# Performance work log

Measured on AMD Instinct MI355X. Metric: run time of the kernel, lower is better.

Reference implementation:

```python
import jax, jax.numpy as jnp
import numpy as np

L, H, DK = 4, 8, 64
NEG = -1e9
PAD = -9999.0


def _ln(z, g, b, eps=1e-6):
    # LayerNormalization: uses unbiased std (torch default) and divides by (std + eps)
    m = jnp.mean(z, axis=-1, keepdims=True)
    s = jnp.std(z, axis=-1, keepdims=True, ddof=1)
    return g * (z - m) / (s + eps) + b


def _mha(q_in, kv_in, w, bw, pw, pb, lnp, mask):
    B, Sq, D = q_in.shape
    q = (q_in @ w[0] + bw[0]).reshape(B, Sq, H, DK).transpose(0, 2, 1, 3)
    k = (kv_in @ w[1] + bw[1]).reshape(B, -1, H, DK).transpose(0, 2, 1, 3)
    v = (kv_in @ w[2] + bw[2]).reshape(B, -1, H, DK).transpose(0, 2, 1, 3)
    scores = jnp.einsum('bhqd,bhkd->bhqk', q, k) * (1.0 / np.sqrt(DK))
    if mask is not None:
        scores = jnp.where(mask[:, None, :, :], NEG, scores)
    attn = jax.nn.softmax(scores, axis=-1)
    ctx = jnp.einsum('bhqk,bhkd->bhqd', attn, v).transpose(0, 2, 1, 3).reshape(B, Sq, H * DK)
    return _ln(q_in + ctx @ pw + pb, lnp[0], lnp[1])


def _ffn(x, w1, b1, w2, b2, lnp):
    # kernel-1 conv1d == pointwise linear; w1:[d_ff,d_model], w2:[d_model,d_ff]
    h = jax.nn.relu(jnp.einsum('bsd,fd->bsf', x, w1) + b1)
    o = jnp.einsum('bsf,df->bsd', h, w2) + b2
    return _ln(x + o, lnp[0], lnp[1])


def _forward(enc_inputs, dec_inputs, emb_w, emb_b, pos_table,
             e_qkv_w, e_qkv_b, e_pw, e_pb, e_ln1, e_w1, e_b1, e_w2, e_b2, e_ln2,
             ds_qkv_w, ds_qkv_b, ds_pw, ds_pb, d_ln1,
             dc_qkv_w, dc_qkv_b, dc_pw, dc_pb, d_ln2,
             d_w1, d_b1, d_w2, d_b2, d_ln3):
    B, Se, F = enc_inputs.shape
    Sd = dec_inputs.shape[1]
    # ConvEmbeddingLayer: kernel-1 conv producing (d_model - n_features) channels, concat with raw inputs
    enc = jnp.concatenate([enc_inputs, jnp.einsum('bsf,of->bso', enc_inputs, emb_w) + emb_b], axis=-1)
    dec = jnp.concatenate([dec_inputs, jnp.einsum('bsf,of->bso', dec_inputs, emb_w) + emb_b], axis=-1)
    # PosEncoding with full lengths -> rows 1..S of the padded table
    enc = enc + pos_table[1:Se + 1]
    dec = dec + pos_table[1:Sd + 1]
    # masks per get_attn_pad_mask / get_attn_subsequent_mask
    enc_pad = jnp.sum(enc_inputs, axis=-1) <= PAD  # [B,Se]
    dec_pad = jnp.sum(dec_inputs, axis=-1) <= PAD  # [B,Sd]
    enc_mask = jnp.broadcast_to(enc_pad[:, None, :], (B, Se, Se))
    causal = jnp.triu(jnp.ones((Sd, Sd), dtype=bool), 1)
    dec_self_mask = jnp.broadcast_to(dec_pad[:, None, :], (B, Sd, Sd)) | causal
    cross_mask = jnp.broadcast_to(enc_pad[:, None, :], (B, Sd, Se))
    for i in range(L):
        enc = _mha(enc, enc, e_qkv_w[i], e_qkv_b[i], e_pw[i], e_pb[i], e_ln1[i], enc_mask)
        enc = _ffn(enc, e_w1[i], e_b1[i], e_w2[i], e_b2[i], e_ln2[i])
    for i in range(L):
        dec = _mha(dec, dec, ds_qkv_w[i], ds_qkv_b[i], ds_pw[i], ds_pb[i], d_ln1[i], dec_self_mask)
        dec = _mha(dec, enc, dc_qkv_w[i], dc_qkv_b[i], dc_pw[i], dc_pb[i], d_ln2[i], cross_mask)
        dec = _ffn(dec, d_w1[i], d_b1[i], d_w2[i], d_b2[i], d_ln3[i])
    return dec


def setup_inputs() -> dict:
    B, Se, Sd, F, Dm, Dff = 8, 512, 512, 32, 512, 2048
    key = jax.random.key(0)
    ks = iter(jax.random.split(key, 32))
    s = 0.02

    def n(shape, sc=s):
        return jax.random.normal(next(ks), shape, jnp.float32) * sc

    # sinusoidal PosEncoding table with leading pad row
    pos = np.arange(Se, dtype=np.float64)[:, None]
    j = np.arange(Dm)[None, :]
    ang = pos / np.power(10000.0, 2.0 * (j // 2) / Dm)
    ang[:, 0::2] = np.sin(ang[:, 0::2])
    ang[:, 1::2] = np.cos(ang[:, 1::2])
    pos_table = jnp.asarray(np.concatenate([np.zeros((1, Dm)), ang]).astype(np.float32))

    ln = jnp.broadcast_to(jnp.stack([jnp.ones(Dm), jnp.zeros(Dm)]), (L, 2, Dm)).astype(jnp.float32) + 0.0
    return {
        'enc_inputs': jax.random.normal(next(ks), (B, Se, F), jnp.float32),
        'dec_inputs': jax.random.normal(next(ks), (B, Sd, F), jnp.float32),
        'emb_w': n((Dm - F, F)), 'emb_b': jnp.zeros(Dm - F, jnp.float32),
        'pos_table': pos_table,
        'e_qkv_w': n((L, 3, Dm, H * DK)), 'e_qkv_b': jnp.zeros((L, 3, H * DK), jnp.float32),
        'e_pw': n((L, H * DK, Dm)), 'e_pb': jnp.zeros((L, Dm), jnp.float32), 'e_ln1': ln,
        'e_w1': n((L, Dff, Dm)), 'e_b1': jnp.zeros((L, Dff), jnp.float32),
        'e_w2': n((L, Dm, Dff)), 'e_b2': jnp.zeros((L, Dm), jnp.float32), 'e_ln2': ln,
        'ds_qkv_w': n((L, 3, Dm, H * DK)), 'ds_qkv_b': jnp.zeros((L, 3, H * DK), jnp.float32),
        'ds_pw': n((L, H * DK, Dm)), 'ds_pb': jnp.zeros((L, Dm), jnp.float32), 'd_ln1': ln,
        'dc_qkv_w': n((L, 3, Dm, H * DK)), 'dc_qkv_b': jnp.zeros((L, 3, H * DK), jnp.float32),
        'dc_pw': n((L, H * DK, Dm)), 'dc_pb': jnp.zeros((L, Dm), jnp.float32), 'd_ln2': ln,
        'd_w1': n((L, Dff, Dm)), 'd_b1': jnp.zeros((L, Dff), jnp.float32),
        'd_w2': n((L, Dm, Dff)), 'd_b2': jnp.zeros((L, Dm), jnp.float32), 'd_ln3': ln,
    }


def reference(enc_inputs, dec_inputs, emb_w, emb_b, pos_table,
              e_qkv_w, e_qkv_b, e_pw, e_pb, e_ln1, e_w1, e_b1, e_w2, e_b2, e_ln2,
              ds_qkv_w, ds_qkv_b, ds_pw, ds_pb, d_ln1,
              dc_qkv_w, dc_qkv_b, dc_pw, dc_pb, d_ln2,
              d_w1, d_b1, d_w2, d_b2, d_ln3):
    return _forward(enc_inputs, dec_inputs, emb_w, emb_b, pos_table,
                    e_qkv_w, e_qkv_b, e_pw, e_pb, e_ln1, e_w1, e_b1, e_w2, e_b2, e_ln2,
                    ds_qkv_w, ds_qkv_b, ds_pw, ds_pb, d_ln1,
                    dc_qkv_w, dc_qkv_b, dc_pw, dc_pb, d_ln2,
                    d_w1, d_b1, d_w2, d_b2, d_ln3)
```

## Files before the change

kernel.cpp:

```cpp
#include <hip/hip_runtime.h>
#include <cstdint>
#include <cstddef>

typedef unsigned short u16;
typedef __bf16 bf16x8 __attribute__((ext_vector_type(8)));
typedef float f32x4 __attribute__((ext_vector_type(4)));

constexpr int Bz = 8, Sq = 512, Hh = 8, DKd = 64, Dm = 512, Dff = 2048, NL = 4;
constexpr int TOK = Bz * Sq;
constexpr size_t MAT = (size_t)512 * 512;
constexpr size_t EL  = (size_t)TOK * Dm;
constexpr size_t WFT = (size_t)Dff * Dm;

__device__ __forceinline__ float bf2f(u16 u) {
  union { uint32_t i; float f; } v; v.i = (uint32_t)u << 16; return v.f;
}
__device__ __forceinline__ u16 f2bf(float f) {
  union { float f; uint32_t i; } v; v.f = f;
  uint32_t i = v.i;
  i += 0x7fffu + ((i >> 16) & 1u);
  return (u16)(i >> 16);
}

__device__ __forceinline__ void gload16(const u16* g, u16* l) {
  __builtin_amdgcn_global_load_lds(
      (const __attribute__((address_space(1))) unsigned int*)g,
      (__attribute__((address_space(3))) unsigned int*)l, 16, 0, 0);
}

template<int BM, int BN, int TAG>
__global__ __launch_bounds__(256)
void gemm_tile(const u16* __restrict__ A, const u16* __restrict__ Bt,
               const float* __restrict__ bias, u16* __restrict__ C,
               int K, int lda, long long sA, int ldb, long long sB,
               int ldc, long long sC, int cmode, int relu, int colofs,
               const u16* A2, int xsplit, const float* __restrict__ posp)
{
  constexpr int HM = BM / 2, HN = BN / 2, MI = HM / 16, NI = HN / 16;
  __shared__ __align__(16) u16 As[BM * 64];
  __shared__ __align__(16) u16 Bs[BN * 64];
  const int bz = blockIdx.z;
  const u16* Abase = A;
  int colbase;
  if (A2 && (int)blockIdx.x >= xsplit) {
    Abase = A2;
    colbase = 512 + ((int)blockIdx.x - xsplit) * BN;
  } else {
    colbase = colofs + (int)blockIdx.x * BN;
  }
  const u16* Ab = Abase + (size_t)bz * (size_t)sA + (size_t)(blockIdx.y * BM) * lda;
  const u16* Bb = Bt + (size_t)bz * (size_t)sB + (size_t)colbase * ldb;
  const int tid  = threadIdx.x;
  const int lane = tid & 63;
  const int wid  = tid >> 6;
  const int l15  = lane & 15;
  const int quad = lane >> 4;
  const int wm   = wid >> 1, wn = wid & 1;

  f32x4 acc[MI][NI] = {};

  for (int k0 = 0; k0 < K; k0 += 64) {
#pragma unroll
    for (int i = 0; i < BM / 32; ++i) {
      const int s = tid + i * 256;
      const int row = s >> 3, c = (s & 7) ^ (row & 7);
      gload16(Ab + (size_t)row * lda + k0 + c * 8, As + s * 8);
    }
#pragma unroll
    for (int i = 0; i < BN / 32; ++i) {
      const int s = tid + i * 256;
      const int row = s >> 3, c = (s & 7) ^ (row & 7);
      gload16(Bb + (size_t)row * ldb + k0 + c * 8, Bs + s * 8);
    }
    __syncthreads();
#pragma unroll
    for (int kk = 0; kk < 2; ++kk) {
      bf16x8 af[MI], bfr[NI];
#pragma unroll
      for (int mi = 0; mi < MI; ++mi) {
        const int ra = wm * HM + mi * 16 + l15;
        af[mi] = *(const bf16x8*)(As + ra * 64 + (((kk * 4 + quad) ^ (ra & 7))) * 8);
      }
#pragma unroll
      for (int ni = 0; ni < NI; ++ni) {
        const int rb = wn * HN + ni * 16 + l15;
        bfr[ni] = *(const bf16x8*)(Bs + rb * 64 + (((kk * 4 + quad) ^ (rb & 7))) * 8);
      }
#pragma unroll
      for (int mi = 0; mi < MI; ++mi)
#pragma unroll
        for (int ni = 0; ni < NI; ++ni)
          acc[mi][ni] = __builtin_amdgcn_mfma_f32_16x16x32_bf16(af[mi], bfr[ni], acc[mi][ni], 0, 0, 0);
    }
    __syncthreads();
  }

  const int rblk = blockIdx.y * BM + wm * HM + quad * 4;
  bool dorepack = false;
  if constexpr (TAG == 0) dorepack = (cmode == 4 && colbase >= 1024);
  if (!dorepack) {
#pragma unroll
    for (int ni = 0; ni < NI; ++ni) {
      const int colx = colbase + wn * HN + ni * 16 + l15;
      const float bv = bias ? bias[colx] : 0.f;
#pragma unroll
      for (int mi = 0; mi < MI; ++mi) {
#pragma unroll
        for (int r = 0; r < 4; ++r) {
          float v = acc[mi][ni][r] + bv;
          if (relu) v = fmaxf(v, 0.f);
          const int grow = rblk + mi * 16 + r;
          size_t off;
          if (cmode == 0) {
            off = (size_t)bz * (size_t)sC + (size_t)grow * ldc + colx;
          } else if (cmode == 5) {
            const int s = grow & 511;
            v += posp[(size_t)(s + 1) * 512 + colx];
            off = (size_t)grow * 512 + colx;
          } else {
            const int sec = colx >> 9, n = colx & 511, h = n >> 6, d = n & 63;
            const int b = grow >> 9, s = grow & 511;
            if (sec == 0) v *= 0.125f;
            off = (size_t)sec * EL + (size_t)b * 262144 + (size_t)h * 32768 + (size_t)s * 64 + d;
          }
          C[off] = f2bf(v);
        }
      }
    }
  } else {
    if constexpr (TAG == 0) {
      u16* Ls = Bs;
#pragma unroll
      for (int ni = 0; ni < NI; ++ni) {
        const int col = wn * HN + ni * 16 + l15;
        const float bv = bias ? bias[colbase + col] : 0.f;
#pragma unroll
        for (int mi = 0; mi < MI; ++mi) {
#pragma unroll
          for (int r = 0; r < 4; ++r) {
            const int srow = wm * HM + mi * 16 + quad * 4 + r;
            Ls[col * 64 + (srow ^ ((col & 7) << 3))] = f2bf(acc[mi][ni][r] + bv);
          }
        }
      }
      __syncthreads();
      const int gb = (blockIdx.y * BM) >> 9, s0 = (blockIdx.y * BM) & 511;
      const int grp = tid >> 3, sl = tid & 7;
      u16* vdst = C + 2 * EL + (size_t)gb * 262144 + s0;
#pragma unroll
      for (int j = 0; j < BN / 32; ++j) {
        const int col = j * 32 + grp;
        const int n = (colbase - 1024) + col, h = n >> 6, d = n & 63;
        uint4 w = *(const uint4*)(Ls + col * 64 + ((sl ^ (col & 7)) << 3));
        *(uint4*)(vdst + (size_t)h * 32768 + (size_t)d * 512 + sl * 8) = w;
      }
    }
  }
}

__global__ __launch_bounds__(256)
void flash_attn(const u16* __restrict__ q, const u16* __restrict__ k,
                const u16* __restrict__ v, const unsigned char* __restrict__ pad,
                u16* __restrict__ ctx, int mtype)
{
  __shared__ __align__(16) u16 KVs[8192];
  __shared__ __align__(16) u16 Pw[4][2048];
  const int bh = blockIdx.y, b = bh >> 3, h = bh & 7;
  const int qt = blockIdx.x;
  const int tid = threadIdx.x, lane = tid & 63, wid = tid >> 6;
  const int l15 = lane & 15, quad = lane >> 4;
  const size_t bho = (size_t)bh * 32768;
  const int qrow = qt * 64 + wid * 16 + l15;
  const int qcd  = qt * 64 + wid * 16 + quad * 4;

  unsigned char* Ps = (unsigned char*)&Pw[0][0];
  if (tid < 128) ((uchar4*)Ps)[tid] = ((const uchar4*)(pad + b * 512))[tid];

  bf16x8 aq0 = *(const bf16x8*)(q + bho + (size_t)qrow * 64 + quad * 8);
  bf16x8 aq1 = *(const bf16x8*)(q + bho + (size_t)qrow * 64 + 32 + quad * 8);

  f32x4 S[32];
#pragma unroll
  for (int kc = 0; kc < 4; ++kc) {
    __syncthreads();
#pragma unroll
    for (int i = 0; i < 4; ++i) {
      const int s = tid + i * 256;
      const int row = s >> 3, c = (s & 7) ^ (row & 7);
      gload16(k + bho + (size_t)(kc * 128 + row) * 64 + c * 8, KVs + s * 8);
    }
    __syncthreads();
#pragma unroll
    for (int t = 0; t < 8; ++t) {
      const int sw = l15 & 7;
      bf16x8 b0 = *(const bf16x8*)(KVs + (t * 16 + l15) * 64 + (quad ^ sw) * 8);
      bf16x8 b1 = *(const bf16x8*)(KVs + (t * 16 + l15) * 64 + ((4 + quad) ^ sw) * 8);
      f32x4 z = {0.f, 0.f, 0.f, 0.f};
      z = __builtin_amdgcn_mfma_f32_16x16x32_bf16(aq0, b0, z, 0, 0, 0);
      S[kc * 8 + t] = __builtin_amdgcn_mfma_f32_16x16x32_bf16(aq1, b1, z, 0, 0, 0);
    }
  }

  unsigned pm = 0u;
#pragma unroll
  for (int t = 0; t < 32; ++t) pm |= (unsigned)(Ps[t * 16 + l15] != 0) << t;

  float inv[4];
#pragma unroll
  for (int r = 0; r < 4; ++r) {
    const int qg = qcd + r;
    float mx = -3.0e38f;
#pragma unroll
    for (int t = 0; t < 32; ++t) {
      const int col = t * 16 + l15;
      const bool m = ((pm >> t) & 1u) || (mtype == 1 && col > qg);
      const float val = m ? -1e9f : S[t][r];
      S[t][r] = val;
      mx = fmaxf(mx, val);
    }
#pragma unroll
    for (int o = 8; o > 0; o >>= 1) mx = fmaxf(mx, __shfl_xor(mx, o));
    float sm = 0.f;
#pragma unroll
    for (int t = 0; t < 32; ++t) { const float e = __expf(S[t][r] - mx); S[t][r] = e; sm += e; }
#pragma unroll
    for (int o = 8; o > 0; o >>= 1) sm += __shfl_xor(sm, o);
    inv[r] = 1.f / sm;
  }

  f32x4 O[4] = {};
  u16* myP = &Pw[wid][0];
#pragma unroll
  for (int kc = 0; kc < 4; ++kc) {
    __syncthreads();
#pragma unroll
    for (int i = 0; i < 4; ++i) {
      const int s = tid + i * 256;
      const int row = s >> 4, c = (s & 15) ^ (row & 15);
      gload16(v + bho + (size_t)row * 512 + kc * 128 + c * 8, KVs + s * 8);
    }
#pragma unroll
    for (int t = 0; t < 8; ++t)
#pragma unroll
      for (int r = 0; r < 4; ++r) {
        const int rowq = quad * 4 + r;
        const int c = 2 * t + (l15 >> 3);
        myP[rowq * 128 + (c ^ rowq) * 8 + (l15 & 7)] = f2bf(S[kc * 8 + t][r] * inv[r]);
      }
    __syncthreads();
#pragma unroll
    for (int kk = 0; kk < 4; ++kk) {
      bf16x8 ap = *(const bf16x8*)(myP + l15 * 128 + ((kk * 4 + quad) ^ l15) * 8);
#pragma unroll
      for (int ni = 0; ni < 4; ++ni) {
        bf16x8 bv = *(const bf16x8*)(KVs + (ni * 16 + l15) * 128 + ((kk * 4 + quad) ^ l15) * 8);
        O[ni] = __builtin_amdgcn_mfma_f32_16x16x32_bf16(ap, bv, O[ni], 0, 0, 0);
      }
    }
  }

  const int token = b * 512 + qcd;
#pragma unroll
  for (int ni = 0; ni < 4; ++ni)
#pragma unroll
    for (int r = 0; r < 4; ++r)
      ctx[(size_t)(token + r) * 512 + h * 64 + ni * 16 + l15] = f2bf(O[ni][r]);
}

__global__ __launch_bounds__(256)
void prep_weights(const float* __restrict__ s0, const float* __restrict__ s1,
                  const float* __restrict__ s2, const float* __restrict__ s3,
                  const float* __restrict__ s4, const float* __restrict__ s5,
                  u16* __restrict__ outT,
                  const float* __restrict__ c0, const float* __restrict__ c1,
                  const float* __restrict__ c2, const float* __restrict__ c3,
                  u16* __restrict__ outC,
                  const float* __restrict__ ew, const float* __restrict__ eb,
                  u16* __restrict__ ewb, float* __restrict__ biasE,
                  const float* __restrict__ xe, const float* __restrict__ xd,
                  u16* __restrict__ xbf,
                  unsigned char* __restrict__ pe, unsigned char* __restrict__ pd)
{
  __shared__ float tile[32][33];
  const int z = blockIdx.z;
  const int tid = threadIdx.y * 32 + threadIdx.x;
  const int r  = tid >> 3;
  const int c4 = (tid & 7) * 4;
  if (z < 48) {
    const float* src; int zi;
    if      (z < 12) { src = s0; zi = z; }
    else if (z < 24) { src = s1; zi = z - 12; }
    else if (z < 36) { src = s2; zi = z - 24; }
    else if (z < 40) { src = s3; zi = z - 36; }
    else if (z < 44) { src = s4; zi = z - 40; }
    else             { src = s5; zi = z - 44; }
    const float* in = src + (size_t)zi * MAT;
    u16* o = outT + (size_t)z * MAT;
    float4 v = *(const float4*)(in + (size_t)(blockIdx.y * 32 + r) * 512 + blockIdx.x * 32 + c4);
    tile[r][c4 + 0] = v.x; tile[r][c4 + 1] = v.y;
    tile[r][c4 + 2] = v.z; tile[r][c4 + 3] = v.w;
    __syncthreads();
    ushort4 w;
    w.x = f2bf(tile[c4 + 0][r]);
    w.y = f2bf(tile[c4 + 1][r]);
    w.z = f2bf(tile[c4 + 2][r]);
    w.w = f2bf(tile[c4 + 3][r]);
    *(ushort4*)(o + (size_t)(blockIdx.x * 32 + r) * 512 + blockIdx.y * 32 + c4) = w;
  } else if (z < 80) {
    const int L = (z - 48) * 256 + blockIdx.y * 16 + blockIdx.x;
    const size_t e0 = ((size_t)L * 256 + tid) * 8;
    const int tens = (int)(e0 >> 22);
    const size_t local = e0 & (4 * WFT - 1);
    const float* srcs[4] = { c0, c1, c2, c3 };
    const float* src = srcs[tens];
    float4 v0 = *(const float4*)(src + local);
    float4 v1 = *(const float4*)(src + local + 4);
    ushort4 ua = { f2bf(v0.x), f2bf(v0.y), f2bf(v0.z), f2bf(v0.w) };
    ushort4 ub = { f2bf(v1.x), f2bf(v1.y), f2bf(v1.z), f2bf(v1.w) };
    uint4 w;
    w.x = (uint32_t)ua.x | ((uint32_t)ua.y << 16);
    w.y = (uint32_t)ua.z | ((uint32_t)ua.w << 16);
    w.z = (uint32_t)ub.x | ((uint32_t)ub.y << 16);
    w.w = (uint32_t)ub.z | ((uint32_t)ub.w << 16);
    *(uint4*)(outC + (size_t)tens * (4 * WFT) + local) = w;
  } else if (z == 80) {
    const int bxy = blockIdx.y * 16 + blockIdx.x;
    if (tid < 128) {
      const int row = bxy * 2 + (tid >> 6);
      const int c = tid & 63;
      float v;
      if (row < 32) v = (c == row) ? 1.f : 0.f;
      else          v = (c < 32) ? ew[(size_t)(row - 32) * 32 + c] : 0.f;
      ewb[(size_t)row * 64 + c] = f2bf(v);
    }
    if (bxy == 0) {
#pragma unroll
      for (int rep = 0; rep < 2; ++rep) {
        const int i = tid + rep * 256;
        biasE[i] = (i < 32) ? 0.f : eb[i - 32];
      }
    }
  } else {
    const int bxy = blockIdx.y * 16 + blockIdx.x;
    const int lw = tid & 31;
#pragma unroll
    for (int rep = 0; rep < 4; ++rep) {
      const int rr0 = bxy * 32 + rep * 8 + (tid >> 5);
      const float* xsrc = (rr0 < 4096) ? xe : xd;
      const int rr = rr0 & 4095;
      const float v = xsrc[(size_t)rr * 32 + lw];
      float sm = v;
#pragma unroll
      for (int o = 16; o > 0; o >>= 1) sm += __shfl_xor(sm, o);
      if (lw == 0) {
        unsigned char* pv = (rr0 < 4096) ? pe : pd;
        pv[rr] = (sm <= -9999.f) ? 1 : 0;
      }
      u16* orow = xbf + (size_t)rr0 * 64;
      orow[lw] = f2bf(v);
      orow[32 + lw] = 0;
    }
  }
}

__global__ __launch_bounds__(256)
void add_ln(const u16* __restrict__ x, const u16* __restrict__ y,
            const float* __restrict__ g, const float* __restrict__ bb,
            u16* __restrict__ out, float* __restrict__ out32)
{
  const int row  = blockIdx.x * 4 + (threadIdx.x >> 6);
  const int lane = threadIdx.x & 63;
  const int c0 = lane * 8;
  const size_t base = (size_t)row * Dm + c0;

  uint4 xr = *(const uint4*)(x + base);
  uint4 yr = *(const uint4*)(y + base);
  const u16* xh = (const u16*)&xr;
  const u16* yh = (const u16*)&yr;
  float z[8];
  float s = 0.f;
#pragma unroll
  for (int j = 0; j < 8; ++j) { z[j] = bf2f(xh[j]) + bf2f(yh[j]); s += z[j]; }
#pragma unroll
  for (int off = 32; off > 0; off >>= 1) s += __shfl_xor(s, off);
  const float mean = s * (1.f / 512.f);
  float ss = 0.f;
#pragma unroll
  for (int j = 0; j < 8; ++j) { z[j] -= mean; ss += z[j] * z[j]; }
#pragma unroll
  for (int off = 32; off > 0; off >>= 1) ss += __shfl_xor(ss, off);
  const float stdv = sqrtf(ss * (1.f / 511.f));
  const float inv = 1.f / (stdv + 1e-6f);

  float4 g0 = *(const float4*)(g + c0),  g1 = *(const float4*)(g + c0 + 4);
  float4 b0 = *(const float4*)(bb + c0), b1 = *(const float4*)(bb + c0 + 4);
  float gv[8] = { g0.x, g0.y, g0.z, g0.w, g1.x, g1.y, g1.z, g1.w };
  float bv[8] = { b0.x, b0.y, b0.z, b0.w, b1.x, b1.y, b1.z, b1.w };
  float o[8];
#pragma unroll
  for (int j = 0; j < 8; ++j) o[j] = gv[j] * z[j] * inv + bv[j];
  if (out32) {
    float4 w0 = { o[0], o[1], o[2], o[3] };
    float4 w1 = { o[4], o[5], o[6], o[7] };
    *(float4*)(out32 + base) = w0;
    *(float4*)(out32 + base + 4) = w1;
  } else {
    uint4 ow;
    u16* oh = (u16*)&ow;
#pragma unroll
    for (int j = 0; j < 8; ++j) oh[j] = f2bf(o[j]);
    *(uint4*)(out + base) = ow;
  }
}

extern "C" void kernel_launch(void* const* d_in, const int* in_sizes, int n_in,
                              void* d_out, int out_size, void* d_ws, size_t ws_size,
                              hipStream_t stream)
{
  (void)in_sizes; (void)n_in; (void)out_size;
  const float* enc_in   = (const float*)d_in[0];
  const float* dec_in   = (const float*)d_in[1];
  const float* emb_w    = (const float*)d_in[2];
  const float* emb_b    = (const float*)d_in[3];
  const float* pos      = (const float*)d_in[4];
  const float* e_qkv_w  = (const float*)d_in[5];
  const float* e_qkv_b  = (const float*)d_in[6];
  const float* e_pw     = (const float*)d_in[7];
  const float* e_pb     = (const float*)d_in[8];
  const float* e_ln1    = (const float*)d_in[9];
  const float* e_w1     = (const float*)d_in[10];
  const float* e_b1     = (const float*)d_in[11];
  const float* e_w2     = (const float*)d_in[12];
  const float* e_b2     = (const float*)d_in[13];
  const float* e_ln2    = (const float*)d_in[14];
  const float* ds_qkv_w = (const float*)d_in[15];
  const float* ds_qkv_b = (const float*)d_in[16];
  const float* ds_pw    = (const float*)d_in[17];
  const float* ds_pb    = (const float*)d_in[18];
  const float* d_ln1    = (const float*)d_in[19];
  const float* dc_qkv_w = (const float*)d_in[20];
  const float* dc_qkv_b = (const float*)d_in[21];
  const float* dc_pw    = (const float*)d_in[22];
  const float* dc_pb    = (const float*)d_in[23];
  const float* d_ln2    = (const float*)d_in[24];
  const float* d_w1     = (const float*)d_in[25];
  const float* d_b1     = (const float*)d_in[26];
  const float* d_w2     = (const float*)d_in[27];
  const float* d_b2     = (const float*)d_in[28];
  const float* d_ln3    = (const float*)d_in[29];

  u16* ws  = (u16*)d_ws;
  u16* enc = ws;
  u16* dec = ws + EL;
  u16* qb  = ws + 2 * EL;
  u16* kb  = ws + 3 * EL;
  u16* vT  = ws + 4 * EL;
  u16* ctx = ws + 5 * EL;
  u16* t1  = ws + 6 * EL;
  u16* hff = ws + 7 * EL;
  u16* wT  = ws + 15 * EL;
  unsigned char* padE = (unsigned char*)(ws + 21 * EL);
  unsigned char* padD = padE + TOK;
  u16* xbf   = ws + 21 * EL + 8192;
  u16* ewb   = xbf + (size_t)8192 * 64;
  float* biasE = (float*)(ewb + 32768);
  u16* wfAll = ws + 22 * EL;
  if (ws_size < 30 * EL * 2 + 2 * TOK) return;

  prep_weights<<<dim3(16, 16, 82), dim3(32, 8), 0, stream>>>(
      e_qkv_w, ds_qkv_w, dc_qkv_w, e_pw, ds_pw, dc_pw, wT,
      e_w1, e_w2, d_w1, d_w2, wfAll,
      emb_w, emb_b, ewb, biasE,
      enc_in, dec_in, xbf, padE, padD);
  gemm_tile<64, 128, 4><<<dim3(4, 128, 1), 256, 0, stream>>>(
      xbf, ewb, biasE, enc, 64, 64, 0, 64, 0, 512, 0, 5, 0, 0, nullptr, 0, pos);

  auto attention = [&](const u16* qsrc, const u16* kvsrc, const u16* wq3, const float* b3,
                       const u16* pwT, const float* pb, const float* ln,
                       const unsigned char* pad, int mtype, u16* x) {
    if (qsrc == kvsrc) {
      gemm_tile<64, 128, 0><<<dim3(12, 64, 1), 256, 0, stream>>>(
          qsrc, wq3, b3, qb, 512, 512, 0, 512, 0, 0, 0, 4, 0, 0, nullptr, 0, nullptr);
    } else {
      gemm_tile<64, 128, 0><<<dim3(12, 64, 1), 256, 0, stream>>>(
          qsrc, wq3, b3, qb, 512, 512, 0, 512, 0, 0, 0, 4, 0, 0, kvsrc, 4, nullptr);
    }
    flash_attn<<<dim3(8, 64), 256, 0, stream>>>(qb, kb, vT, pad, ctx, mtype);
    gemm_tile<64, 64, 1><<<dim3(8, 64, 1), 256, 0, stream>>>(
        ctx, pwT, pb, t1, 512, 512, 0, 512, 0, 512, 0, 0, 0, 0, nullptr, 0, nullptr);
    add_ln<<<TOK / 4, 256, 0, stream>>>(x, t1, ln, ln + 512, x, nullptr);
  };

  auto ffn = [&](u16* x, const u16* w1b, const float* b1, const u16* w2b,
                 const float* b2, const float* ln, float* o32) {
    gemm_tile<128, 128, 2><<<dim3(16, 32, 1), 256, 0, stream>>>(
        x, w1b, b1, hff, 512, 512, 0, 512, 0, 2048, 0, 0, 1, 0, nullptr, 0, nullptr);
    gemm_tile<64, 64, 3><<<dim3(8, 64, 1), 256, 0, stream>>>(
        hff, w2b, b2, t1, 2048, 2048, 0, 2048, 0, 512, 0, 0, 0, 0, nullptr, 0, nullptr);
    add_ln<<<TOK / 4, 256, 0, stream>>>(x, t1, ln, ln + 512, x, o32);
  };

  for (int i = 0; i < NL; ++i) {
    attention(enc, enc, wT + (size_t)(i * 3) * MAT, e_qkv_b + i * 3 * 512,
              wT + (size_t)(36 + i) * MAT, e_pb + i * 512, e_ln1 + i * 1024, padE, 0, enc);
    ffn(enc, wfAll + (size_t)i * WFT, e_b1 + i * Dff,
        wfAll + 4 * WFT + (size_t)i * WFT, e_b2 + i * Dm, e_ln2 + i * 1024, nullptr);
  }

  for (int i = 0; i < NL; ++i) {
    attention(dec, dec, wT + (size_t)(12 + i * 3) * MAT, ds_qkv_b + i * 3 * 512,
              wT + (size_t)(40 + i) * MAT, ds_pb + i * 512, d_ln1 + i * 1024, padD, 1, dec);
    attention(dec, enc, wT + (size_t)(24 + i * 3) * MAT, dc_qkv_b + i * 3 * 512,
              wT + (size_t)(44 + i) * MAT, dc_pb + i * 512, d_ln2 + i * 1024, padE, 2, dec);
    ffn(dec, wfAll + 8 * WFT + (size_t)i * WFT, d_b1 + i * Dff,
        wfAll + 12 * WFT + (size_t)i * WFT, d_b2 + i * Dm, d_ln3 + i * 1024,
        (i == NL - 1) ? (float*)d_out : nullptr);
  }
}
```

Baseline: 1.275 ms.

## Read K/V directly from global in flash attention and shrink FFN1 tile

Flash attention stops staging K and V through shared memory and loads MFMA operands straight from global memory (relying on cache), which removes the LDS buffer and several barriers and frees LDS for occupancy. The GEMM kernel drops unused batch-stride and column-offset parameters, and the first FFN GEMM switches from 128x128 to 64x128 tiles with twice the row blocks. Uncoalesced global reads per MFMA step may raise memory traffic and latency, and the V read pattern is strided.

Result: slower. 1.479 ms (+16.0%).

```diff
diff --git a/kernel.cpp b/kernel.cpp
--- a/kernel.cpp
+++ b/kernel.cpp
@@ -32,24 +32,19 @@
 __global__ __launch_bounds__(256)
 void gemm_tile(const u16* __restrict__ A, const u16* __restrict__ Bt,
                const float* __restrict__ bias, u16* __restrict__ C,
-               int K, int lda, long long sA, int ldb, long long sB,
-               int ldc, long long sC, int cmode, int relu, int colofs,
+               int K, int lda, int ldb, int ldc, int cmode, int relu,
                const u16* A2, int xsplit, const float* __restrict__ posp)
 {
   constexpr int HM = BM / 2, HN = BN / 2, MI = HM / 16, NI = HN / 16;
   __shared__ __align__(16) u16 As[BM * 64];
   __shared__ __align__(16) u16 Bs[BN * 64];
-  const int bz = blockIdx.z;
+  const int bx = blockIdx.x, by = blockIdx.y;
   const u16* Abase = A;
   int colbase;
-  if (A2 && (int)blockIdx.x >= xsplit) {
-    Abase = A2;
-    colbase = 512 + ((int)blockIdx.x - xsplit) * BN;
-  } else {
-    colbase = colofs + (int)blockIdx.x * BN;
-  }
-  const u16* Ab = Abase + (size_t)bz * (size_t)sA + (size_t)(blockIdx.y * BM) * lda;
-  const u16* Bb = Bt + (size_t)bz * (size_t)sB + (size_t)colbase * ldb;
+  if (A2 && bx >= xsplit) { Abase = A2; colbase = 512 + (bx - xsplit) * BN; }
+  else                    { colbase = bx * BN; }
+  const u16* Ab = Abase + (size_t)(by * BM) * lda;
+  const u16* Bb = Bt + (size_t)colbase * ldb;
   const int tid  = threadIdx.x;
   const int lane = tid & 63;
   const int wid  = tid >> 6;
@@ -95,7 +90,7 @@
     __syncthreads();
   }
 
-  const int rblk = blockIdx.y * BM + wm * HM + quad * 4;
+  const int rblk = by * BM + wm * HM + quad * 4;
   bool dorepack = false;
   if constexpr (TAG == 0) dorepack = (cmode == 4 && colbase >= 1024);
   if (!dorepack) {
@@ -112,7 +107,7 @@
           const int grow = rblk + mi * 16 + r;
           size_t off;
           if (cmode == 0) {
-            off = (size_t)bz * (size_t)sC + (size_t)grow * ldc + colx;
+            off = (size_t)grow * ldc + colx;
           } else if (cmode == 5) {
             const int s = grow & 511;
             v += posp[(size_t)(s + 1) * 512 + colx];
@@ -144,7 +139,7 @@
         }
       }
       __syncthreads();
-      const int gb = (blockIdx.y * BM) >> 9, s0 = (blockIdx.y * BM) & 511;
+      const int gb = (by * BM) >> 9, s0 = (by * BM) & 511;
       const int grp = tid >> 3, sl = tid & 7;
       u16* vdst = C + 2 * EL + (size_t)gb * 262144 + s0;
 #pragma unroll
@@ -163,8 +158,8 @@
                 const u16* __restrict__ v, const unsigned char* __restrict__ pad,
                 u16* __restrict__ ctx, int mtype)
 {
-  __shared__ __align__(16) u16 KVs[8192];
   __shared__ __align__(16) u16 Pw[4][2048];
+  __shared__ unsigned char Ps[512];
   const int bh = blockIdx.y, b = bh >> 3, h = bh & 7;
   const int qt = blockIdx.x;
   const int tid = threadIdx.x, lane = tid & 63, wid = tid >> 6;
@@ -173,7 +168,6 @@
   const int qrow = qt * 64 + wid * 16 + l15;
   const int qcd  = qt * 64 + wid * 16 + quad * 4;
 
-  unsigned char* Ps = (unsigned char*)&Pw[0][0];
   if (tid < 128) ((uchar4*)Ps)[tid] = ((const uchar4*)(pad + b * 512))[tid];
 
   bf16x8 aq0 = *(const bf16x8*)(q + bho + (size_t)qrow * 64 + quad * 8);
@@ -181,25 +175,15 @@
 
   f32x4 S[32];
 #pragma unroll
-  for (int kc = 0; kc < 4; ++kc) {
-    __syncthreads();
-#pragma unroll
-    for (int i = 0; i < 4; ++i) {
-      const int s = tid + i * 256;
-      const int row = s >> 3, c = (s & 7) ^ (row & 7);
-      gload16(k + bho + (size_t)(kc * 128 + row) * 64 + c * 8, KVs + s * 8);
-    }
-    __syncthreads();
-#pragma unroll
-    for (int t = 0; t < 8; ++t) {
-      const int sw = l15 & 7;
-      bf16x8 b0 = *(const bf16x8*)(KVs + (t * 16 + l15) * 64 + (quad ^ sw) * 8);
-      bf16x8 b1 = *(const bf16x8*)(KVs + (t * 16 + l15) * 64 + ((4 + quad) ^ sw) * 8);
-      f32x4 z = {0.f, 0.f, 0.f, 0.f};
-      z = __builtin_amdgcn_mfma_f32_16x16x32_bf16(aq0, b0, z, 0, 0, 0);
-      S[kc * 8 + t] = __builtin_amdgcn_mfma_f32_16x16x32_bf16(aq1, b1, z, 0, 0, 0);
-    }
-  }
+  for (int t = 0; t < 32; ++t) {
+    const u16* kr = k + bho + (size_t)(t * 16 + l15) * 64 + quad * 8;
+    bf16x8 b0 = *(const bf16x8*)kr;
+    bf16x8 b1 = *(const bf16x8*)(kr + 32);
+    f32x4 z = {0.f, 0.f, 0.f, 0.f};
+    z = __builtin_amdgcn_mfma_f32_16x16x32_bf16(aq0, b0, z, 0, 0, 0);
+    S[t] = __builtin_amdgcn_mfma_f32_16x16x32_bf16(aq1, b1, z, 0, 0, 0);
+  }
+  __syncthreads();
 
   unsigned pm = 0u;
 #pragma unroll
@@ -234,12 +218,6 @@
   for (int kc = 0; kc < 4; ++kc) {
     __syncthreads();
 #pragma unroll
-    for (int i = 0; i < 4; ++i) {
-      const int s = tid + i * 256;
-      const int row = s >> 4, c = (s & 15) ^ (row & 15);
-      gload16(v + bho + (size_t)row * 512 + kc * 128 + c * 8, KVs + s * 8);
-    }
-#pragma unroll
     for (int t = 0; t < 8; ++t)
 #pragma unroll
       for (int r = 0; r < 4; ++r) {
@@ -253,7 +231,8 @@
       bf16x8 ap = *(const bf16x8*)(myP + l15 * 128 + ((kk * 4 + quad) ^ l15) * 8);
 #pragma unroll
       for (int ni = 0; ni < 4; ++ni) {
-        bf16x8 bv = *(const bf16x8*)(KVs + (ni * 16 + l15) * 128 + ((kk * 4 + quad) ^ l15) * 8);
+        bf16x8 bv = *(const bf16x8*)(v + bho + (size_t)(ni * 16 + l15) * 512 +
+                                     kc * 128 + (kk * 4 + quad) * 8);
         O[ni] = __builtin_amdgcn_mfma_f32_16x16x32_bf16(ap, bv, O[ni], 0, 0, 0);
       }
     }
@@ -453,8 +432,6 @@
   u16* enc = ws;
   u16* dec = ws + EL;
   u16* qb  = ws + 2 * EL;
-  u16* kb  = ws + 3 * EL;
-  u16* vT  = ws + 4 * EL;
   u16* ctx = ws + 5 * EL;
   u16* t1  = ws + 6 * EL;
   u16* hff = ws + 7 * EL;
@@ -472,46 +449,47 @@
       e_w1, e_w2, d_w1, d_w2, wfAll,
       emb_w, emb_b, ewb, biasE,
       enc_in, dec_in, xbf, padE, padD);
-  gemm_tile<64, 128, 4><<<dim3(4, 128, 1), 256, 0, stream>>>(
-      xbf, ewb, biasE, enc, 64, 64, 0, 64, 0, 512, 0, 5, 0, 0, nullptr, 0, pos);
-
-  auto attention = [&](const u16* qsrc, const u16* kvsrc, const u16* wq3, const float* b3,
-                       const u16* pwT, const float* pb, const float* ln,
-                       const unsigned char* pad, int mtype, u16* x) {
-    if (qsrc == kvsrc) {
-      gemm_tile<64, 128, 0><<<dim3(12, 64, 1), 256, 0, stream>>>(
-          qsrc, wq3, b3, qb, 512, 512, 0, 512, 0, 0, 0, 4, 0, 0, nullptr, 0, nullptr);
-    } else {
-      gemm_tile<64, 128, 0><<<dim3(12, 64, 1), 256, 0, stream>>>(
-          qsrc, wq3, b3, qb, 512, 512, 0, 512, 0, 0, 0, 4, 0, 0, kvsrc, 4, nullptr);
-    }
-    flash_attn<<<dim3(8, 64), 256, 0, stream>>>(qb, kb, vT, pad, ctx, mtype);
-    gemm_tile<64, 64, 1><<<dim3(8, 64, 1), 256, 0, stream>>>(
-        ctx, pwT, pb, t1, 512, 512, 0, 512, 0, 512, 0, 0, 0, 0, nullptr, 0, nullptr);
+  gemm_tile<64, 128, 4><<<dim3(4, 128), 256, 0, stream>>>(
+      xbf, ewb, biasE, enc, 64, 64, 64, 512, 5, 0, nullptr, 0, pos);
+
+  auto attention = [&](const u16* qsrc, const u16* kvsrc, const u16* wq3,
+                       const float* b3, const u16* pwT, const float* pb,
+                       const float* ln, const unsigned char* pad, int mtype,
+                       u16* x) {
+    const u16* A2 = (qsrc == kvsrc) ? nullptr : kvsrc;
+    gemm_tile<64, 128, 0><<<dim3(12, 64), 256, 0, stream>>>(
+        qsrc, wq3, b3, qb, 512, 512, 512, 0, 4, 0, A2, 4, nullptr);
+    flash_attn<<<dim3(8, 64), 256, 0, stream>>>(qb, qb + EL, qb + 2 * EL,
+                                                pad, ctx, mtype);
+    gemm_tile<64, 64, 1><<<dim3(8, 64), 256, 0, stream>>>(
+        ctx, pwT, pb, t1, 512, 512, 512, 512, 0, 0, nullptr, 0, nullptr);
     add_ln<<<TOK / 4, 256, 0, stream>>>(x, t1, ln, ln + 512, x, nullptr);
   };
 
   auto ffn = [&](u16* x, const u16* w1b, const float* b1, const u16* w2b,
                  const float* b2, const float* ln, float* o32) {
-    gemm_tile<128, 128, 2><<<dim3(16, 32, 1), 256, 0, stream>>>(
-        x, w1b, b1, hff, 512, 512, 0, 512, 0, 2048, 0, 0, 1, 0, nullptr, 0, nullptr);
-    gemm_tile<64, 64, 3><<<dim3(8, 64, 1), 256, 0, stream>>>(
-        hff, w2b, b2, t1, 2048, 2048, 0, 2048, 0, 512, 0, 0, 0, 0, nullptr, 0, nullptr);
+    gemm_tile<64, 128, 2><<<dim3(16, 64), 256, 0, stream>>>(
+        x, w1b, b1, hff, 512, 512, 512, 2048, 0, 1, nullptr, 0, nullptr);
+    gemm_tile<64, 64, 3><<<dim3(8, 64), 256, 0, stream>>>(
+        hff, w2b, b2, t1, 2048, 2048, 2048, 512, 0, 0, nullptr, 0, nullptr);
     add_ln<<<TOK / 4, 256, 0, stream>>>(x, t1, ln, ln + 512, x, o32);
   };
 
   for (int i = 0; i < NL; ++i) {
     attention(enc, enc, wT + (size_t)(i * 3) * MAT, e_qkv_b + i * 3 * 512,
-              wT + (size_t)(36 + i) * MAT, e_pb + i * 512, e_ln1 + i * 1024, padE, 0, enc);
+              wT + (size_t)(36 + i) * MAT, e_pb + i * 512, e_ln1 + i * 1024,
+              padE, 0, enc);
     ffn(enc, wfAll + (size_t)i * WFT, e_b1 + i * Dff,
-        wfAll + 4 * WFT + (size_t)i * WFT, e_b2 + i * Dm, e_ln2 + i * 1024, nullptr);
-  }
-
+        wfAll + 4 * WFT + (size_t)i * WFT, e_b2 + i * Dm, e_ln2 + i * 1024,
+        nullptr);
+  }
   for (int i = 0; i < NL; ++i) {
     attention(dec, dec, wT + (size_t)(12 + i * 3) * MAT, ds_qkv_b + i * 3 * 512,
-              wT + (size_t)(40 + i) * MAT, ds_pb + i * 512, d_ln1 + i * 1024, padD, 1, dec);
+              wT + (size_t)(40 + i) * MAT, ds_pb + i * 512, d_ln1 + i * 1024,
+              padD, 1, dec);
     attention(dec, enc, wT + (size_t)(24 + i * 3) * MAT, dc_qkv_b + i * 3 * 512,
-              wT + (size_t)(44 + i) * MAT, dc_pb + i * 512, d_ln2 + i * 1024, padE, 2, dec);
+              wT + (size_t)(44 + i) * MAT, dc_pb + i * 512, d_ln2 + i * 1024,
+              padE, 2, dec);
     ffn(dec, wfAll + 8 * WFT + (size_t)i * WFT, d_b1 + i * Dff,
         wfAll + 12 * WFT + (size_t)i * WFT, d_b2 + i * Dm, d_ln3 + i * 1024,
         (i == NL - 1) ? (float*)d_out : nullptr);
```
